# Kernel tuning notes

Measured on AMD Instinct MI355X. Metric: run time of the kernel, lower is better.

Reference implementation:

```python
import jax, jax.numpy as jnp
import numpy as np

BS, N, M, D = 8, 2048, 64, 1024
N_WAY, N_SHOT = 64, 5


def setup_inputs() -> dict:
    key = jax.random.key(0)
    k1, k2, k3, k4, k5 = jax.random.split(key, 5)
    return {
        "prototypes": jax.random.normal(k1, (BS, M, D), dtype=jnp.float32),
        "masktypes": jax.random.uniform(k2, (BS, M, D), dtype=jnp.float32),
        "query": jax.random.normal(k3, (BS, N, D), dtype=jnp.float32),
        "support": jax.random.normal(k4, (BS, N_WAY * N_SHOT, D), dtype=jnp.float32),
        "support_labels": jax.random.randint(k5, (BS, N_WAY * N_SHOT), 0, N_WAY, dtype=jnp.int64),
        "scale": jnp.ones((1,), dtype=jnp.float32),
        "n_way": N_WAY,
        "n_shot": N_SHOT,
    }


def reference(prototypes, masktypes, query, support, support_labels, scale, n_way, n_shot):
    # Masked squared Euclidean distance:
    #   logits[b,n,m] = sum_d (mask[b,m,d] * (query[b,n,d] - proto[b,m,d]))^2
    # Expanded via the GEMM trick to avoid the (bs,n,m,d) intermediate:
    #   = sum_d mask^2 q^2 - 2 sum_d q (mask^2 p) + sum_d (mask p)^2
    dims = prototypes.shape[-1]
    mask2 = masktypes * masktypes                       # [b,m,d]
    q_term = jnp.einsum('bnd,bmd->bnm', query * query, mask2)
    cross = jnp.einsum('bnd,bmd->bnm', query, mask2 * prototypes)
    mp = masktypes * prototypes                         # [b,m,d]
    p_term = jnp.sum(mp * mp, axis=-1)[:, None, :]      # [b,1,m]
    logits = (q_term - 2.0 * cross + p_term) / dims     # normalize=True
    return scale * logits
```

## Files before the change

kernel.cpp:

```cpp
#include <hip/hip_runtime.h>

#define BSZ 8
#define NQ 2048
#define MP 64
#define DD 1024
#define BN 64
#define BK 64
#define K2 128
#define LDK 136
#define KT 16

typedef __bf16 bf16x8 __attribute__((ext_vector_type(8)));
typedef float f32x4 __attribute__((ext_vector_type(4)));
typedef unsigned short us8 __attribute__((ext_vector_type(8)));

__device__ __forceinline__ unsigned short f2bf(float f) {
    union { float f; unsigned int u; } v; v.f = f;
    unsigned int u = v.u;
    return (unsigned short)((u + 0x7FFFu + ((u >> 16) & 1u)) >> 16);
}

__global__ __launch_bounds__(256) void proto_head_kernel(
    const float* __restrict__ proto,
    const float* __restrict__ mask,
    const float* __restrict__ query,
    const float* __restrict__ scale,
    float* __restrict__ out)
{
    __shared__ unsigned short Qs[BN][LDK];
    __shared__ unsigned short Ps[MP][LDK];
    __shared__ float Pterm[MP];

    const int tid = threadIdx.x;
    const int bid = blockIdx.x;
    const int b  = bid & 7;
    const int n0 = (bid >> 3) * BN;

    if (tid < MP) Pterm[tid] = 0.0f;

    const int qr = tid >> 4;
    const int qc = tid & 15;
    const int pm = tid >> 2;
    const int pc = tid & 3;

    const float* qbase = query + ((size_t)b * NQ + n0) * DD;
    const float* mrow  = mask  + ((size_t)(b * MP + pm)) * DD;
    const float* prow  = proto + ((size_t)(b * MP + pm)) * DD;

    const int lane = tid & 63;
    const int wid  = tid >> 6;
    const int lrow = lane & 15;
    const int lq8  = (lane >> 4) * 8;

    f32x4 acc[4];
    acc[0] = acc[1] = acc[2] = acc[3] = (f32x4){0.f, 0.f, 0.f, 0.f};
    float pacc = 0.f;

    float4 qv[4], mv[4], pv[4];

    {
        #pragma unroll
        for (int p = 0; p < 4; ++p)
            qv[p] = *(const float4*)(qbase + (size_t)(qr + 16 * p) * DD + 4 * qc);
        #pragma unroll
        for (int p = 0; p < 4; ++p) {
            const int d4 = pc + 4 * p;
            mv[p] = *(const float4*)(mrow + 4 * d4);
            pv[p] = *(const float4*)(prow + 4 * d4);
        }
    }

    for (int kt = 0; kt < KT; ++kt) {
        #pragma unroll
        for (int p = 0; p < 4; ++p) {
            const float4 q = qv[p];
            us8 o;
            o[0] = f2bf(q.x * q.x); o[1] = f2bf(q.x);
            o[2] = f2bf(q.y * q.y); o[3] = f2bf(q.y);
            o[4] = f2bf(q.z * q.z); o[5] = f2bf(q.z);
            o[6] = f2bf(q.w * q.w); o[7] = f2bf(q.w);
            *(us8*)(&Qs[qr + 16 * p][8 * qc]) = o;
        }
        #pragma unroll
        for (int p = 0; p < 4; ++p) {
            const int d4 = pc + 4 * p;
            const float4 mk = mv[p], pr = pv[p];
            const float m2x = mk.x * mk.x, m2y = mk.y * mk.y,
                        m2z = mk.z * mk.z, m2w = mk.w * mk.w;
            const float ax = mk.x * pr.x, ay = mk.y * pr.y,
                        az = mk.z * pr.z, aw = mk.w * pr.w;
            pacc += ax * ax + ay * ay + az * az + aw * aw;
            us8 o;
            o[0] = f2bf(m2x); o[1] = f2bf(-2.f * m2x * pr.x);
            o[2] = f2bf(m2y); o[3] = f2bf(-2.f * m2y * pr.y);
            o[4] = f2bf(m2z); o[5] = f2bf(-2.f * m2z * pr.z);
            o[6] = f2bf(m2w); o[7] = f2bf(-2.f * m2w * pr.w);
            *(us8*)(&Ps[pm][8 * d4]) = o;
        }
        __syncthreads();

        if (kt + 1 < KT) {
            const float* qp = qbase + (kt + 1) * BK;
            #pragma unroll
            for (int p = 0; p < 4; ++p)
                qv[p] = *(const float4*)(qp + (size_t)(qr + 16 * p) * DD + 4 * qc);
            const float* mp2 = mrow + (kt + 1) * BK;
            const float* pp2 = prow + (kt + 1) * BK;
            #pragma unroll
            for (int p = 0; p < 4; ++p) {
                const int d4 = pc + 4 * p;
                mv[p] = *(const float4*)(mp2 + 4 * d4);
                pv[p] = *(const float4*)(pp2 + 4 * d4);
            }
        }

        #pragma unroll
        for (int k0 = 0; k0 < K2; k0 += 32) {
            const bf16x8 a = *(const bf16x8*)(&Qs[16 * wid + lrow][k0 + lq8]);
            #pragma unroll
            for (int mi = 0; mi < 4; ++mi) {
                const bf16x8 bb = *(const bf16x8*)(&Ps[16 * mi + lrow][k0 + lq8]);
                acc[mi] = __builtin_amdgcn_mfma_f32_16x16x32_bf16(a, bb, acc[mi], 0, 0, 0);
            }
        }
        __syncthreads();
    }

    atomicAdd(&Pterm[pm], pacc);
    __syncthreads();

    const float sc = scale[0] * (1.0f / (float)DD);
    #pragma unroll
    for (int mi = 0; mi < 4; ++mi) {
        const int m = 16 * mi + lrow;
        const float pt = Pterm[m];
        const size_t obase =
            ((size_t)b * NQ + (size_t)(n0 + 16 * wid + (lane >> 4) * 4)) * MP + m;
        #pragma unroll
        for (int r = 0; r < 4; ++r)
            out[obase + (size_t)r * MP] = (acc[mi][r] + pt) * sc;
    }
}

extern "C" void kernel_launch(void* const* d_in, const int* in_sizes, int n_in,
                              void* d_out, int out_size, void* d_ws, size_t ws_size,
                              hipStream_t stream) {
    (void)in_sizes; (void)n_in; (void)d_ws; (void)ws_size; (void)out_size;
    const float* proto = (const float*)d_in[0];
    const float* mask  = (const float*)d_in[1];
    const float* query = (const float*)d_in[2];
    const float* scale = (const float*)d_in[5];
    float* out = (float*)d_out;

    dim3 grid(BSZ * (NQ / BN));
    proto_head_kernel<<<grid, dim3(256), 0, stream>>>(proto, mask, query, scale, out);
}
```

Measured before the change: 133.3 us.

## Precompute packed prototype operand in separate kernel and shrink query tiles

Adds a pack kernel that converts mask and prototype rows into a bf16 interleaved operand and per-row p-term once, stored in workspace. The main kernel then streams the packed operand directly from global/L2 into registers instead of recomputing it in every block, and uses 16-row query tiles with double-buffered LDS and register prefetch. This removes redundant per-block mask/prototype reads and conversion work. In exchange it adds a second launch and rereads of the packed buffer from L2 by every block.

```diff
diff --git a/kernel.cpp b/kernel.cpp
--- a/kernel.cpp
+++ b/kernel.cpp
@@ -4,11 +4,13 @@
 #define NQ 2048
 #define MP 64
 #define DD 1024
-#define BN 64
+#define K2ALL 2048
+#define BN 16
 #define BK 64
 #define K2 128
 #define LDK 136
 #define KT 16
+#define NTILES (NQ / BN)
 
 typedef __bf16 bf16x8 __attribute__((ext_vector_type(8)));
 typedef float f32x4 __attribute__((ext_vector_type(4)));
@@ -20,138 +22,131 @@
     return (unsigned short)((u + 0x7FFFu + ((u >> 16) & 1u)) >> 16);
 }
 
-__global__ __launch_bounds__(256) void proto_head_kernel(
+__global__ __launch_bounds__(256) void pack_kernel(
     const float* __restrict__ proto,
     const float* __restrict__ mask,
+    unsigned short* __restrict__ Pp,
+    float* __restrict__ Pterm)
+{
+    const int row = blockIdx.x;
+    const int t = threadIdx.x;
+
+    const float4 mk = *(const float4*)(mask  + (size_t)row * DD + 4 * t);
+    const float4 pr = *(const float4*)(proto + (size_t)row * DD + 4 * t);
+
+    const float m2x = mk.x * mk.x, m2y = mk.y * mk.y,
+                m2z = mk.z * mk.z, m2w = mk.w * mk.w;
+    const float ax = mk.x * pr.x, ay = mk.y * pr.y,
+                az = mk.z * pr.z, aw = mk.w * pr.w;
+    float pacc = ax * ax + ay * ay + az * az + aw * aw;
+
+    us8 o;
+    o[0] = f2bf(m2x); o[1] = f2bf(-2.f * m2x * pr.x);
+    o[2] = f2bf(m2y); o[3] = f2bf(-2.f * m2y * pr.y);
+    o[4] = f2bf(m2z); o[5] = f2bf(-2.f * m2z * pr.z);
+    o[6] = f2bf(m2w); o[7] = f2bf(-2.f * m2w * pr.w);
+    *(us8*)(Pp + (size_t)row * K2ALL + 8 * t) = o;
+
+    __shared__ float red[4];
+    #pragma unroll
+    for (int off = 32; off > 0; off >>= 1)
+        pacc += __shfl_down(pacc, off, 64);
+    const int lane = t & 63, w = t >> 6;
+    if (lane == 0) red[w] = pacc;
+    __syncthreads();
+    if (t == 0) Pterm[row] = red[0] + red[1] + red[2] + red[3];
+}
+
+__global__ __launch_bounds__(256, 4) void proto_main_kernel(
     const float* __restrict__ query,
+    const unsigned short* __restrict__ Pp,
+    const float* __restrict__ Pterm,
     const float* __restrict__ scale,
     float* __restrict__ out)
 {
-    __shared__ unsigned short Qs[BN][LDK];
-    __shared__ unsigned short Ps[MP][LDK];
-    __shared__ float Pterm[MP];
+    __shared__ unsigned short Qs[2][BN][LDK];
 
     const int tid = threadIdx.x;
     const int bid = blockIdx.x;
     const int b  = bid & 7;
     const int n0 = (bid >> 3) * BN;
 
-    if (tid < MP) Pterm[tid] = 0.0f;
-
-    const int qr = tid >> 4;
-    const int qc = tid & 15;
-    const int pm = tid >> 2;
-    const int pc = tid & 3;
-
-    const float* qbase = query + ((size_t)b * NQ + n0) * DD;
-    const float* mrow  = mask  + ((size_t)(b * MP + pm)) * DD;
-    const float* prow  = proto + ((size_t)(b * MP + pm)) * DD;
+    const int qrow = tid >> 4;
+    const int qc   = tid & 15;
+    const float* qptr = query + ((size_t)b * NQ + n0 + qrow) * DD + 4 * qc;
 
     const int lane = tid & 63;
     const int wid  = tid >> 6;
     const int lrow = lane & 15;
-    const int lq8  = (lane >> 4) * 8;
+    const int lq   = (lane >> 4) * 8;
 
-    f32x4 acc[4];
-    acc[0] = acc[1] = acc[2] = acc[3] = (f32x4){0.f, 0.f, 0.f, 0.f};
-    float pacc = 0.f;
+    const int mcol = 16 * wid + lrow;
+    const unsigned short* bptr = Pp + ((size_t)(b * MP + mcol)) * K2ALL + lq;
 
-    float4 qv[4], mv[4], pv[4];
+    f32x4 acc = (f32x4){0.f, 0.f, 0.f, 0.f};
+    float4 q[2];
+    bf16x8 bv[2][4];
 
-    {
+    const float pt = Pterm[b * MP + mcol];
+    const float sc = scale[0] * (1.0f / (float)DD);
+
+    q[0] = *(const float4*)(qptr);
+    q[1] = *(const float4*)(qptr + BK);
+    #pragma unroll
+    for (int i = 0; i < 4; ++i)
+        bv[0][i] = *(const bf16x8*)(bptr + 32 * i);
+
+    #pragma unroll
+    for (int kt = 0; kt < KT; ++kt) {
+        const int cur = kt & 1;
+
+        {
+            const float4 qq = q[cur];
+            us8 o;
+            o[0] = f2bf(qq.x * qq.x); o[1] = f2bf(qq.x);
+            o[2] = f2bf(qq.y * qq.y); o[3] = f2bf(qq.y);
+            o[4] = f2bf(qq.z * qq.z); o[5] = f2bf(qq.z);
+            o[6] = f2bf(qq.w * qq.w); o[7] = f2bf(qq.w);
+            *(us8*)(&Qs[cur][qrow][8 * qc]) = o;
+        }
+        __syncthreads();
+
+        if (kt + 2 < KT)
+            q[cur] = *(const float4*)(qptr + (kt + 2) * BK);
+        if (kt + 1 < KT) {
+            #pragma unroll
+            for (int i = 0; i < 4; ++i)
+                bv[(kt + 1) & 1][i] =
+                    *(const bf16x8*)(bptr + (kt + 1) * K2 + 32 * i);
+        }
+
         #pragma unroll
-        for (int p = 0; p < 4; ++p)
-            qv[p] = *(const float4*)(qbase + (size_t)(qr + 16 * p) * DD + 4 * qc);
-        #pragma unroll
-        for (int p = 0; p < 4; ++p) {
-            const int d4 = pc + 4 * p;
-            mv[p] = *(const float4*)(mrow + 4 * d4);
-            pv[p] = *(const float4*)(prow + 4 * d4);
+        for (int i = 0; i < 4; ++i) {
+            const bf16x8 a = *(const bf16x8*)(&Qs[cur][lrow][32 * i + lq]);
+            acc = __builtin_amdgcn_mfma_f32_16x16x32_bf16(a, bv[cur][i], acc, 0, 0, 0);
         }
     }
 
-    for (int kt = 0; kt < KT; ++kt) {
-        #pragma unroll
-        for (int p = 0; p < 4; ++p) {
-            const float4 q = qv[p];
-            us8 o;
-            o[0] = f2bf(q.x * q.x); o[1] = f2bf(q.x);
-            o[2] = f2bf(q.y * q.y); o[3] = f2bf(q.y);
-            o[4] = f2bf(q.z * q.z); o[5] = f2bf(q.z);
-            o[6] = f2bf(q.w * q.w); o[7] = f2bf(q.w);
-            *(us8*)(&Qs[qr + 16 * p][8 * qc]) = o;
-        }
-        #pragma unroll
-        for (int p = 0; p < 4; ++p) {
-            const int d4 = pc + 4 * p;
-            const float4 mk = mv[p], pr = pv[p];
-            const float m2x = mk.x * mk.x, m2y = mk.y * mk.y,
-                        m2z = mk.z * mk.z, m2w = mk.w * mk.w;
-            const float ax = mk.x * pr.x, ay = mk.y * pr.y,
-                        az = mk.z * pr.z, aw = mk.w * pr.w;
-            pacc += ax * ax + ay * ay + az * az + aw * aw;
-            us8 o;
-            o[0] = f2bf(m2x); o[1] = f2bf(-2.f * m2x * pr.x);
-            o[2] = f2bf(m2y); o[3] = f2bf(-2.f * m2y * pr.y);
-            o[4] = f2bf(m2z); o[5] = f2bf(-2.f * m2z * pr.z);
-            o[6] = f2bf(m2w); o[7] = f2bf(-2.f * m2w * pr.w);
-            *(us8*)(&Ps[pm][8 * d4]) = o;
-        }
-        __syncthreads();
-
-        if (kt + 1 < KT) {
-            const float* qp = qbase + (kt + 1) * BK;
-            #pragma unroll
-            for (int p = 0; p < 4; ++p)
-                qv[p] = *(const float4*)(qp + (size_t)(qr + 16 * p) * DD + 4 * qc);
-            const float* mp2 = mrow + (kt + 1) * BK;
-            const float* pp2 = prow + (kt + 1) * BK;
-            #pragma unroll
-            for (int p = 0; p < 4; ++p) {
-                const int d4 = pc + 4 * p;
-                mv[p] = *(const float4*)(mp2 + 4 * d4);
-                pv[p] = *(const float4*)(pp2 + 4 * d4);
-            }
-        }
-
-        #pragma unroll
-        for (int k0 = 0; k0 < K2; k0 += 32) {
-            const bf16x8 a = *(const bf16x8*)(&Qs[16 * wid + lrow][k0 + lq8]);
-            #pragma unroll
-            for (int mi = 0; mi < 4; ++mi) {
-                const bf16x8 bb = *(const bf16x8*)(&Ps[16 * mi + lrow][k0 + lq8]);
-                acc[mi] = __builtin_amdgcn_mfma_f32_16x16x32_bf16(a, bb, acc[mi], 0, 0, 0);
-            }
-        }
-        __syncthreads();
-    }
-
-    atomicAdd(&Pterm[pm], pacc);
-    __syncthreads();
-
-    const float sc = scale[0] * (1.0f / (float)DD);
+    const size_t ob = ((size_t)b * NQ + (size_t)(n0 + (lane >> 4) * 4)) * MP + mcol;
     #pragma unroll
-    for (int mi = 0; mi < 4; ++mi) {
-        const int m = 16 * mi + lrow;
-        const float pt = Pterm[m];
-        const size_t obase =
-            ((size_t)b * NQ + (size_t)(n0 + 16 * wid + (lane >> 4) * 4)) * MP + m;
-        #pragma unroll
-        for (int r = 0; r < 4; ++r)
-            out[obase + (size_t)r * MP] = (acc[mi][r] + pt) * sc;
-    }
+    for (int r = 0; r < 4; ++r)
+        out[ob + (size_t)r * MP] = (acc[r] + pt) * sc;
 }
 
 extern "C" void kernel_launch(void* const* d_in, const int* in_sizes, int n_in,
                               void* d_out, int out_size, void* d_ws, size_t ws_size,
                               hipStream_t stream) {
-    (void)in_sizes; (void)n_in; (void)d_ws; (void)ws_size; (void)out_size;
+    (void)in_sizes; (void)n_in; (void)ws_size; (void)out_size;
     const float* proto = (const float*)d_in[0];
     const float* mask  = (const float*)d_in[1];
     const float* query = (const float*)d_in[2];
     const float* scale = (const float*)d_in[5];
     float* out = (float*)d_out;
 
-    dim3 grid(BSZ * (NQ / BN));
-    proto_head_kernel<<<grid, dim3(256), 0, stream>>>(proto, mask, query, scale, out);
+    unsigned short* Pp = (unsigned short*)d_ws;
+    float* Pterm = (float*)((char*)d_ws + (size_t)BSZ * MP * K2ALL * 2);
+
+    pack_kernel<<<dim3(BSZ * MP), dim3(256), 0, stream>>>(proto, mask, Pp, Pterm);
+    proto_main_kernel<<<dim3(BSZ * NTILES), dim3(256), 0, stream>>>(
+        query, Pp, Pterm, scale, out);
 }
```

Result: slower. 140.5 us (+5.4%).
